# Kernel tuning notes

Hardware: AMD Instinct MI355X
Metric: run time of the kernel (lower is better)

The kernel has to match this reference:

```python
import jax, jax.numpy as jnp
import numpy as np

E = 3_200_000  # edges
N = 100_000    # atoms
B = 64         # graphs


def setup_inputs() -> dict:
    key = jax.random.key(0)
    k1, k2, k3, k4 = jax.random.split(key, 4)
    disp = jax.random.normal(k1, (E, 3), dtype=jnp.float32)
    edge_w = jax.random.uniform(k2, (E,), dtype=jnp.float32)
    edge_index = jax.random.randint(k3, (2, E), 0, N)
    batch = jnp.sort(jax.random.randint(k4, (N,), 0, B))
    return {"disp": disp, "edge_w": edge_w, "edge_index": edge_index,
            "batch": batch, "num_graphs": B}


def reference(disp, edge_w, edge_index, batch, num_graphs):
    n_atoms = batch.shape[0]

    # Surrogate differentiable energy of disp (stands in for the upstream model):
    # E = sum_e w_e * ||disp_e||^2. pairwise_force = -dE/ddisp via autodiff,
    # matching torch.autograd.grad(energy, disp).
    def energy_fn(d):
        return jnp.sum(edge_w * jnp.sum(d * d, axis=-1))

    pairwise_force = -jax.grad(energy_fn)(disp)  # (E, 3)

    # Per-edge virial outer product: (E, 3, 3)
    virial_e = disp[:, :, None] * pairwise_force[:, None, :]

    # Double scatter-add to atoms (both endpoints), then scatter to graphs.
    v_atom = (jax.ops.segment_sum(virial_e, edge_index[0], num_segments=n_atoms)
              + jax.ops.segment_sum(virial_e, edge_index[1], num_segments=n_atoms))  # (N,3,3)
    v_graph = jax.ops.segment_sum(v_atom, batch, num_segments=num_graphs)  # (B,3,3)
    return v_graph
```

## Files before the change

### kernel.cpp

```cpp
#include <hip/hip_runtime.h>
#include <hip/hip_fp8.h>


#define NG 64
#define NCOMP 6
#define NPART (NG * NCOMP)
#define RED1_BLOCKS 64
#define MFMA_BLOCKS 1024
#define WPB 4
#define MROWB 80
#define DROWB 80
#define DTROWS 6

typedef unsigned char  u8_t;
typedef unsigned int   u32_t;
typedef __attribute__((ext_vector_type(2))) long long long2_t;
typedef __attribute__((ext_vector_type(4))) float f32x4;

__device__ __forceinline__ int eperm(int e) {
    return (((e >> 3) & 3) << 4) | (((e >> 5) & 1) << 3) | (e & 7);
}

__device__ __forceinline__ u8_t f2fp8(float f) {
    return (u8_t)__hip_cvt_float_to_fp8(f, __HIP_SATFINITE, __HIP_E4M3);
}

__device__ __forceinline__ void lds_add(float* p, float v) {
    __hip_atomic_fetch_add(p, v, __ATOMIC_RELAXED, __HIP_MEMORY_SCOPE_WORKGROUP);
}

__device__ __forceinline__ int gsearch(const int* Bs, int a) {
    int lo = 0;
#pragma unroll
    for (int st = 32; st >= 1; st >>= 1)
        lo += (Bs[lo + st] <= a) ? st : 0;
    return lo;
}

__global__ void bounds_build(const int* __restrict__ batch, int* __restrict__ B,
                             int N)
{
    int g = threadIdx.x;
    if (g > 64) return;
    int lo = 0, len = N;
    while (len > 0) {
        int half = len >> 1;
        int mid  = lo + half;
        if (batch[mid] < g) { lo = mid + 1; len -= half + 1; }
        else                { len = half; }
    }
    B[g] = lo;
}

__global__ __launch_bounds__(256) void virial_mfma(
    const float* __restrict__ disp, const float* __restrict__ edge_w,
    const int* __restrict__ edge_index, const int* __restrict__ Bg,
    float* __restrict__ partials, int E)
{
    __shared__ u8_t Msh[WPB][NG * MROWB];
    __shared__ u8_t Dsh[WPB][DTROWS * DROWB];
    __shared__ int  Bs[65];

    const int lane = threadIdx.x & 63;
    const int wave = threadIdx.x >> 6;
    u8_t* Mw = Msh[wave];
    u8_t* Dw = Dsh[wave];

    if (threadIdx.x < 65) Bs[threadIdx.x] = Bg[threadIdx.x];
    {
        u32_t* p = (u32_t*)Mw;
        for (int i = lane; i < NG * MROWB / 4; i += 64) p[i] = 0u;
        u32_t* q = (u32_t*)Dw;
        for (int i = lane; i < DTROWS * DROWB / 4; i += 64) q[i] = 0u;
    }
    __syncthreads();

    f32x4 acc0 = {0,0,0,0}, acc1 = {0,0,0,0}, acc2 = {0,0,0,0}, acc3 = {0,0,0,0};
    const int ngroups = (E + 63) >> 6;
    const int gstride = (int)gridDim.x * WPB;
    const int c_l  = lane & 15;
    const int k4   = lane >> 4;
    const int mcol = eperm(lane);
    const int drow = (c_l < DTROWS) ? c_l : (DTROWS - 1);
    int pg0 = 0, pg1 = 0;

    int grp = (int)blockIdx.x * WPB + wave;

    float pw = 0.f, px = 0.f, py = 0.f, pz = 0.f;
    int   ps = 0, pt = 0;
    if (grp < ngroups) {
        int e  = grp * 64 + lane;
        int ec = e < E ? e : E - 1;
        pw = (e < E) ? edge_w[ec] : 0.f;
        px = disp[ec * 3 + 0];
        py = disp[ec * 3 + 1];
        pz = disp[ec * 3 + 2];
        ps = edge_index[ec];
        pt = edge_index[E + ec];
    }

    while (grp < ngroups) {
        const float w = pw, d0 = px, d1 = py, d2 = pz;
        const int   sC = ps, tC = pt;

        const int nxt = grp + gstride;
        if (nxt < ngroups) {
            int e  = nxt * 64 + lane;
            int ec = e < E ? e : E - 1;
            pw = (e < E) ? edge_w[ec] : 0.f;
            px = disp[ec * 3 + 0];
            py = disp[ec * 3 + 1];
            pz = disp[ec * 3 + 2];
            ps = edge_index[ec];
            pt = edge_index[E + ec];
        }

        const int g0 = gsearch(Bs, sC);
        const int g1 = gsearch(Bs, tC);

        Mw[pg0 * MROWB + mcol] = 0;
        Mw[pg1 * MROWB + mcol] = 0;
        Mw[g0 * MROWB + mcol] = 0x38u;
        Mw[g1 * MROWB + mcol] = (g1 == g0) ? 0x40u : 0x38u;
        pg0 = g0; pg1 = g1;

        float cw = -2.f * w;
        Dw[0 * DROWB + mcol] = f2fp8(cw * d0 * d0);
        Dw[1 * DROWB + mcol] = f2fp8(cw * d0 * d1);
        Dw[2 * DROWB + mcol] = f2fp8(cw * d0 * d2);
        Dw[3 * DROWB + mcol] = f2fp8(cw * d1 * d1);
        Dw[4 * DROWB + mcol] = f2fp8(cw * d1 * d2);
        Dw[5 * DROWB + mcol] = f2fp8(cw * d2 * d2);

        long2_t bf = *(const long2_t*)&Dw[drow * DROWB + k4 * 16];
        long2_t a0 = *(const long2_t*)&Mw[( 0 + c_l) * MROWB + k4 * 16];
        long2_t a1 = *(const long2_t*)&Mw[(16 + c_l) * MROWB + k4 * 16];
        long2_t a2 = *(const long2_t*)&Mw[(32 + c_l) * MROWB + k4 * 16];
        long2_t a3 = *(const long2_t*)&Mw[(48 + c_l) * MROWB + k4 * 16];

        acc0 = __builtin_amdgcn_mfma_f32_16x16x32_fp8_fp8(a0[0], bf[0], acc0, 0, 0, 0);
        acc1 = __builtin_amdgcn_mfma_f32_16x16x32_fp8_fp8(a1[0], bf[0], acc1, 0, 0, 0);
        acc2 = __builtin_amdgcn_mfma_f32_16x16x32_fp8_fp8(a2[0], bf[0], acc2, 0, 0, 0);
        acc3 = __builtin_amdgcn_mfma_f32_16x16x32_fp8_fp8(a3[0], bf[0], acc3, 0, 0, 0);
        acc0 = __builtin_amdgcn_mfma_f32_16x16x32_fp8_fp8(a0[1], bf[1], acc0, 0, 0, 0);
        acc1 = __builtin_amdgcn_mfma_f32_16x16x32_fp8_fp8(a1[1], bf[1], acc1, 0, 0, 0);
        acc2 = __builtin_amdgcn_mfma_f32_16x16x32_fp8_fp8(a2[1], bf[1], acc2, 0, 0, 0);
        acc3 = __builtin_amdgcn_mfma_f32_16x16x32_fp8_fp8(a3[1], bf[1], acc3, 0, 0, 0);

        grp = nxt;
    }

    __syncthreads();
    float* Ow = (float*)Mw;
    if (c_l < NCOMP) {
#pragma unroll
        for (int r = 0; r < 4; ++r) {
            Ow[( 0 + k4 * 4 + r) * NCOMP + c_l] = acc0[r];
            Ow[(16 + k4 * 4 + r) * NCOMP + c_l] = acc1[r];
            Ow[(32 + k4 * 4 + r) * NCOMP + c_l] = acc2[r];
            Ow[(48 + k4 * 4 + r) * NCOMP + c_l] = acc3[r];
        }
    }
    __syncthreads();
    for (int i = threadIdx.x; i < NPART; i += blockDim.x) {
        float s = ((const float*)Msh[0])[i] + ((const float*)Msh[1])[i]
                + ((const float*)Msh[2])[i] + ((const float*)Msh[3])[i];
        partials[(size_t)blockIdx.x * NPART + i] = s;
    }
}

__global__ __launch_bounds__(NPART) void reduce1_kernel(
    const float* __restrict__ partials, float* __restrict__ partials2, int nblk)
{
    int i = threadIdx.x, j = blockIdx.x;
    float s = 0.f;
    for (int b = j; b < nblk; b += RED1_BLOCKS)
        s += partials[(size_t)b * NPART + i];
    partials2[(size_t)j * NPART + i] = s;
}

__global__ __launch_bounds__(NPART) void reduce2_kernel(
    const float* __restrict__ partials2, float* __restrict__ dst)
{
    int i = threadIdx.x;
    float s = 0.f;
#pragma unroll
    for (int j = 0; j < RED1_BLOCKS; ++j)
        s += partials2[(size_t)j * NPART + i];
    int g = i / NCOMP, c = i % NCOMP;
    int r   = (c < 3) ? 0 : ((c < 5) ? 1 : 2);
    int col = (c < 3) ? c : ((c < 5) ? c - 2 : 2);
    dst[g * 9 + r * 3 + col] = s;
    if (r != col) dst[g * 9 + col * 3 + r] = s;
}

__global__ void zero_out_kernel(float* __restrict__ out, int n) {
    int i = blockIdx.x * blockDim.x + threadIdx.x;
    if (i < n) out[i] = 0.f;
}

__global__ __launch_bounds__(256) void virial_atomic(
    const float* __restrict__ disp, const float* __restrict__ edge_w,
    const int* __restrict__ edge_index, const int* __restrict__ batch,
    float* __restrict__ out, int E)
{
    __shared__ float acc[NG * 7];
    for (int i = threadIdx.x; i < NG * 7; i += blockDim.x) acc[i] = 0.f;
    __syncthreads();
    int tid = blockIdx.x * blockDim.x + threadIdx.x;
    int stride = gridDim.x * blockDim.x;
    for (int e = tid; e < E; e += stride) {
        float d0 = disp[e*3], d1 = disp[e*3+1], d2 = disp[e*3+2];
        float c = -2.f * edge_w[e];
        int g0 = batch[edge_index[e]], g1 = batch[edge_index[E + e]];
        float v[6] = {c*d0*d0, c*d0*d1, c*d0*d2, c*d1*d1, c*d1*d2, c*d2*d2};
#pragma unroll
        for (int k = 0; k < 6; ++k) {
            lds_add(&acc[g0*7+k], v[k]);
            lds_add(&acc[g1*7+k], v[k]);
        }
    }
    __syncthreads();
    for (int i = threadIdx.x; i < NG * 9; i += blockDim.x) {
        int g = i / 9, ij = i % 9, r = ij / 3, cc = ij % 3;
        int lo = r < cc ? r : cc, hi = r < cc ? cc : r;
        int comp = (lo == 0) ? hi : ((lo == 1) ? 2 + hi : 5);
        __hip_atomic_fetch_add(&out[i], acc[g*7+comp], __ATOMIC_RELAXED, __HIP_MEMORY_SCOPE_AGENT);
    }
}

extern "C" void kernel_launch(void* const* d_in, const int* in_sizes, int n_in,
                              void* d_out, int out_size, void* d_ws, size_t ws_size,
                              hipStream_t stream) {
    const float* disp       = (const float*)d_in[0];
    const float* edge_w     = (const float*)d_in[1];
    const int*   edge_index = (const int*)d_in[2];
    const int*   batch      = (const int*)d_in[3];
    float*       out        = (float*)d_out;
    const int E = in_sizes[1];
    const int N = in_sizes[3];

    const size_t need = (size_t)(MFMA_BLOCKS + RED1_BLOCKS) * NPART * sizeof(float)
                        + 128 * sizeof(int);

    if (ws_size >= need) {
        float* pm = (float*)d_ws;
        float* p2 = pm + (size_t)MFMA_BLOCKS * NPART;
        int*   B  = (int*)(p2 + (size_t)RED1_BLOCKS * NPART);

        bounds_build<<<1, 128, 0, stream>>>(batch, B, N);
        virial_mfma<<<MFMA_BLOCKS, 256, 0, stream>>>(disp, edge_w, edge_index, B, pm, E);
        reduce1_kernel<<<RED1_BLOCKS, NPART, 0, stream>>>(pm, p2, MFMA_BLOCKS);
        reduce2_kernel<<<1, NPART, 0, stream>>>(p2, out);
    } else {
        zero_out_kernel<<<1, 256, 0, stream>>>(out, NG * 9);
        virial_atomic<<<2048, 256, 0, stream>>>(disp, edge_w, edge_index, batch, out, E);
    }
}
```

Baseline: 38.41 us.

## Fold graph-bounds search into main kernel and use interpolated group lookup

Removes the separate bounds_build launch by having each block of the main kernel binary-search the sorted batch array to fill its shared graph-boundary table. The per-edge graph lookup changes from a fixed 6-step binary search to a guess from a*64/N followed by linear correction steps. This saves one kernel launch and its dependency, but every block now repeats 65 binary searches over global memory at startup. The linear correction loops are cheap only when graph sizes are close to uniform and can diverge within a wave otherwise.

```diff
diff --git a/kernel.cpp b/kernel.cpp
--- a/kernel.cpp
+++ b/kernel.cpp
@@ -29,33 +29,18 @@
     __hip_atomic_fetch_add(p, v, __ATOMIC_RELAXED, __HIP_MEMORY_SCOPE_WORKGROUP);
 }
 
-__device__ __forceinline__ int gsearch(const int* Bs, int a) {
-    int lo = 0;
-#pragma unroll
-    for (int st = 32; st >= 1; st >>= 1)
-        lo += (Bs[lo + st] <= a) ? st : 0;
-    return lo;
-}
-
-__global__ void bounds_build(const int* __restrict__ batch, int* __restrict__ B,
-                             int N)
-{
-    int g = threadIdx.x;
-    if (g > 64) return;
-    int lo = 0, len = N;
-    while (len > 0) {
-        int half = len >> 1;
-        int mid  = lo + half;
-        if (batch[mid] < g) { lo = mid + 1; len -= half + 1; }
-        else                { len = half; }
-    }
-    B[g] = lo;
+__device__ __forceinline__ int gsearch(const int* Bs, int a, float rcpN) {
+    int g = (int)((float)a * rcpN);
+    g = g > 63 ? 63 : g;
+    while (Bs[g] > a) --g;
+    while (Bs[g + 1] <= a) ++g;
+    return g;
 }
 
 __global__ __launch_bounds__(256) void virial_mfma(
     const float* __restrict__ disp, const float* __restrict__ edge_w,
-    const int* __restrict__ edge_index, const int* __restrict__ Bg,
-    float* __restrict__ partials, int E)
+    const int* __restrict__ edge_index, const int* __restrict__ batch,
+    float* __restrict__ partials, int E, int N, float rcpN)
 {
     __shared__ u8_t Msh[WPB][NG * MROWB];
     __shared__ u8_t Dsh[WPB][DTROWS * DROWB];
@@ -66,7 +51,17 @@
     u8_t* Mw = Msh[wave];
     u8_t* Dw = Dsh[wave];
 
-    if (threadIdx.x < 65) Bs[threadIdx.x] = Bg[threadIdx.x];
+    if (threadIdx.x < 65) {
+        int g = threadIdx.x;
+        int lo = 0, len = N;
+        while (len > 0) {
+            int half = len >> 1;
+            int mid  = lo + half;
+            if (batch[mid] < g) { lo = mid + 1; len -= half + 1; }
+            else                { len = half; }
+        }
+        Bs[g] = lo;
+    }
     {
         u32_t* p = (u32_t*)Mw;
         for (int i = lane; i < NG * MROWB / 4; i += 64) p[i] = 0u;
@@ -115,8 +110,8 @@
             pt = edge_index[E + ec];
         }
 
-        const int g0 = gsearch(Bs, sC);
-        const int g1 = gsearch(Bs, tC);
+        const int g0 = gsearch(Bs, sC, rcpN);
+        const int g1 = gsearch(Bs, tC, rcpN);
 
         Mw[pg0 * MROWB + mcol] = 0;
         Mw[pg1 * MROWB + mcol] = 0;
@@ -239,17 +234,16 @@
     float*       out        = (float*)d_out;
     const int E = in_sizes[1];
     const int N = in_sizes[3];
-
-    const size_t need = (size_t)(MFMA_BLOCKS + RED1_BLOCKS) * NPART * sizeof(float)
-                        + 128 * sizeof(int);
+    const float rcpN = (float)NG / (float)N;
+
+    const size_t need = (size_t)(MFMA_BLOCKS + RED1_BLOCKS) * NPART * sizeof(float);
 
     if (ws_size >= need) {
         float* pm = (float*)d_ws;
         float* p2 = pm + (size_t)MFMA_BLOCKS * NPART;
-        int*   B  = (int*)(p2 + (size_t)RED1_BLOCKS * NPART);
-
-        bounds_build<<<1, 128, 0, stream>>>(batch, B, N);
-        virial_mfma<<<MFMA_BLOCKS, 256, 0, stream>>>(disp, edge_w, edge_index, B, pm, E);
+
+        virial_mfma<<<MFMA_BLOCKS, 256, 0, stream>>>(disp, edge_w, edge_index,
+                                                     batch, pm, E, N, rcpN);
         reduce1_kernel<<<RED1_BLOCKS, NPART, 0, stream>>>(pm, p2, MFMA_BLOCKS);
         reduce2_kernel<<<1, NPART, 0, stream>>>(p2, out);
     } else {
```

After: 36.46 us, median of 2. 1.05x faster.
